# Kernel tuning notes

Hardware: AMD Instinct MI355X
Metric: run time of the kernel (lower is better)

The kernel has to match this reference:

```python
import jax, jax.numpy as jnp
import numpy as np
from math import sqrt

MIN_SCORE = 0.05
MAX_OVERLAP = 0.45
TOP_K = 200


def make_priors():
    feature_dims = {'mid': 18, 'end': 9, 'a': 9, 'b': 5, 'c': 3, 'd': 1}
    obj_scales = {'mid': 0.2, 'end': 0.2, 'a': 0.375, 'b': 0.55, 'c': 0.725, 'd': 0.9}
    aspect_ratio = {'mid': [1.0, 2.0, 3.0, 0.5, 0.333], 'end': [1.0, 2.0, 3.0, 0.5, 0.333],
                    'a': [1.0, 2.0, 3.0, 0.5, 0.333], 'b': [1.0, 2.0, 3.0, 0.5, 0.333],
                    'c': [1.0, 2.0, 0.5], 'd': [1.0, 2.0, 0.5]}
    fmaps = list(feature_dims.keys())
    boxes = []
    for k, fmap in enumerate(fmaps):
        for i in range(feature_dims[fmap]):
            for j in range(feature_dims[fmap]):
                cx = (j + 0.5) / feature_dims[fmap]
                cy = (i + 0.5) / feature_dims[fmap]
                for ratio in aspect_ratio[fmap]:
                    boxes.append([cx, cy, obj_scales[fmap] * sqrt(ratio), obj_scales[fmap] / sqrt(ratio)])
                if fmap in ['mid', 'end', 'a', 'b', 'c']:
                    s = sqrt(obj_scales[fmap] * obj_scales[fmaps[k + 1]])
                else:
                    s = 1.0
                boxes.append([cx, cy, s, s])
    return np.clip(np.asarray(boxes, dtype=np.float32), 0.0, 1.0)  # [3106, 4]


def setup_inputs() -> dict:
    key = jax.random.key(0)
    k1, k2 = jax.random.split(key)
    return {
        'predicted_locs': jax.random.normal(k1, (4, 3106, 4), dtype=jnp.float32),
        'predicted_scores': jax.random.normal(k2, (4, 3106, 21), dtype=jnp.float32),
        'priors_cxcy': jnp.asarray(make_priors()),
    }


def _decode(predicted_locs, priors):
    # gcxgcy_to_cxcy then cxcy_to_xy (standard SSD variances 0.1 / 0.2)
    cxcy = predicted_locs[..., :2] * priors[..., 2:] / 10.0 + priors[..., :2]
    wh = jnp.exp(predicted_locs[..., 2:] / 5.0) * priors[..., 2:]
    return jnp.concatenate([cxcy - wh / 2.0, cxcy + wh / 2.0], axis=-1)  # xyxy


def _detect_image(boxes_i, probs_i):
    # boxes_i: [P,4] xyxy, probs_i: [P,C] softmax scores
    P = boxes_i.shape[0]
    C = probs_i.shape[1]
    # full pairwise Jaccard overlap [P,P]
    lt = jnp.maximum(boxes_i[:, None, :2], boxes_i[None, :, :2])
    rb = jnp.minimum(boxes_i[:, None, 2:], boxes_i[None, :, 2:])
    inter = jnp.prod(jnp.clip(rb - lt, 0.0), axis=-1)
    area = jnp.prod(boxes_i[:, 2:] - boxes_i[:, :2], axis=-1)
    iou = inter / (area[:, None] + area[None, :] - inter)

    cls = probs_i[:, 1:].T                      # [C-1, P], skip background
    valid = cls > MIN_SCORE
    order = jnp.argsort(-jnp.where(valid, cls, -jnp.inf), axis=1)  # [C-1, P]
    valid_s = jnp.take_along_axis(valid, order, axis=1)
    iou_sg = jax.lax.stop_gradient(iou)

    def body(i, suppress):                       # greedy NMS over sorted boxes, all classes at once
        bi = order[:, i]                         # [C-1] prior index per class
        rows = jnp.take_along_axis(iou_sg[bi], order, axis=1) > MAX_OVERLAP  # [C-1, P]
        skip = suppress[:, i] | ~valid_s[:, i]
        proc = (suppress | rows).at[:, i].set(False)
        return jnp.where(skip[:, None], suppress, proc)

    suppress = jax.lax.fori_loop(0, P, body, ~valid_s)
    keep = ~suppress                             # [C-1, P] (sorted order)

    scores_s = jnp.take_along_axis(cls, order, axis=1)
    cand_scores = jnp.where(keep, scores_s, -jnp.inf).reshape(-1)     # [(C-1)*P]
    cand_boxes = boxes_i[order].reshape(-1, 4)
    cand_labels = jnp.broadcast_to(jnp.arange(1, C, dtype=jnp.int32)[:, None], (C - 1, P)).reshape(-1)

    top_scores, top_idx = jax.lax.top_k(cand_scores, TOP_K)
    top_boxes = cand_boxes[top_idx]
    top_labels = cand_labels[top_idx]

    has = jnp.isfinite(top_scores)
    top_scores = jnp.where(has, top_scores, 0.0)
    top_boxes = jnp.where(has[:, None], top_boxes, 0.0)
    top_labels = jnp.where(has, top_labels, 0)
    count = jnp.minimum(jnp.sum(keep).astype(jnp.int32), TOP_K)

    # torch fallback: a single background box when nothing is detected
    none = count == 0
    top_boxes = top_boxes.at[0].set(jnp.where(none, jnp.array([0.0, 0.0, 1.0, 1.0], dtype=top_boxes.dtype), top_boxes[0]))
    count = jnp.where(none, jnp.int32(1), count)
    return top_boxes, top_labels, top_scores, count


def reference(predicted_locs, predicted_scores, priors_cxcy):
    probs = jax.nn.softmax(predicted_scores, axis=2)          # [B,P,C]
    boxes = _decode(predicted_locs, priors_cxcy[None])        # [B,P,4]
    all_boxes, all_labels, all_scores, counts = jax.vmap(_detect_image)(boxes, probs)
    return all_boxes, all_labels, all_scores, counts
```

## Files before the change

kernel.cpp:

```cpp
#include <hip/hip_runtime.h>

#define NB 4
#define NPRI 3106
#define NC 21
#define NCLS 20
#define KMAX 200
#define NMAX 1024
#define WMAX 16
#define TMAX (WMAX*(WMAX+1)/2)
#define MIN_SC 0.05f
#define MAX_OV 0.45f

#define F_PROBS 0
#define F_KEYS  (F_PROBS + NB*NCLS*NPRI)
#define F_BOXES (F_KEYS + NB*NCLS*NMAX*2)
#define F_AREAS (F_BOXES + NB*NCLS*NMAX*4)
#define F_NCAND (F_AREAS + NB*NCLS*NMAX)
#define F_M     (F_NCAND + 128)
#define F_POOL  (F_M + NB*NCLS*WMAX*NMAX*2)
#define F_CNT   (F_POOL + NB*NCLS*KMAX*2)
#define F_DONE  (F_CNT + NB*NCLS)

#define OUT_BOXES  0
#define OUT_LABELS (NB*KMAX*4)
#define OUT_SCORES (OUT_LABELS + NB*KMAX)
#define OUT_COUNTS (OUT_SCORES + NB*KMAX)

__device__ __forceinline__ void decode_box(const float* __restrict__ locs,
                                           const float* __restrict__ priors,
                                           int b, int pi,
                                           float& x1, float& y1, float& x2, float& y2) {
    const float* l  = locs + ((size_t)b * NPRI + pi) * 4;
    const float* pr = priors + (size_t)pi * 4;
    float pcx = pr[0], pcy = pr[1], pw = pr[2], ph = pr[3];
    float cx = l[0] * pw / 10.0f + pcx;
    float cy = l[1] * ph / 10.0f + pcy;
    float w  = expf(l[2] / 5.0f) * pw;
    float h  = expf(l[3] / 5.0f) * ph;
    x1 = cx - w / 2.0f;  y1 = cy - h / 2.0f;
    x2 = cx + w / 2.0f;  y2 = cy + h / 2.0f;
}

__device__ __forceinline__ unsigned long long shfl_xor_u64(unsigned long long v, int m) {
    unsigned lo = (unsigned)v, hi = (unsigned)(v >> 32);
    lo = __shfl_xor(lo, m);
    hi = __shfl_xor(hi, m);
    return ((unsigned long long)hi << 32) | lo;
}

__device__ __forceinline__ void softmax_push(const float* __restrict__ v, int c,
                                             int r, unsigned long long* keys,
                                             int* n_sh) {
    float m = -1e30f;
    #pragma unroll
    for (int k = 0; k < NC; ++k) m = fmaxf(m, v[k]);
    float sum = 0.0f, ec = 0.0f;
    #pragma unroll
    for (int k = 0; k < NC; ++k) {
        float e = expf(v[k] - m);
        sum += e;
        if (k == c + 1) ec = e;
    }
    float val = ec / sum;
    if (val > MIN_SC) {
        int idx = atomicAdd(n_sh, 1);
        if (idx < NMAX) {
            unsigned int sb = __float_as_uint(val);
            keys[idx] = ((unsigned long long)(~sb) << 32) | (unsigned int)r;
        }
    }
}

__global__ __launch_bounds__(1024)
void det_prep(const float* __restrict__ scores, const float* __restrict__ locs,
              const float* __restrict__ priors, float* __restrict__ ws) {
    const int bc  = blockIdx.x;
    const int b   = bc / NCLS;
    const int c   = bc - b * NCLS;
    const int tid = threadIdx.x;

    __shared__ unsigned long long keys[NMAX];
    __shared__ int n_sh;
    if (tid == 0) n_sh = 0;
    __syncthreads();

    const float* sbase = scores + (size_t)b * NPRI * NC;
    {
        float v0[NC], v1[NC], v2[NC];
        const float* s0 = sbase + (size_t)(tid)        * NC;
        const float* s1 = sbase + (size_t)(tid + 1024) * NC;
        const float* s2 = sbase + (size_t)(tid + 2048) * NC;
        #pragma unroll
        for (int k = 0; k < NC; ++k) { v0[k] = s0[k]; }
        #pragma unroll
        for (int k = 0; k < NC; ++k) { v1[k] = s1[k]; }
        #pragma unroll
        for (int k = 0; k < NC; ++k) { v2[k] = s2[k]; }
        softmax_push(v0, c, tid,        keys, &n_sh);
        softmax_push(v1, c, tid + 1024, keys, &n_sh);
        softmax_push(v2, c, tid + 2048, keys, &n_sh);
        if (tid < NPRI - 3072) {
            float v3[NC];
            const float* s3 = sbase + (size_t)(tid + 3072) * NC;
            #pragma unroll
            for (int k = 0; k < NC; ++k) { v3[k] = s3[k]; }
            softmax_push(v3, c, tid + 3072, keys, &n_sh);
        }
    }
    __syncthreads();
    int n = n_sh; if (n > NMAX) n = NMAX;

    unsigned long long mykey = (tid < n) ? keys[tid] : ~0ull;
    __syncthreads();
    for (int k = 2; k <= NMAX; k <<= 1) {
        for (int j = k >> 1; j > 0; j >>= 1) {
            unsigned long long other;
            if (j >= 64) {
                keys[tid] = mykey;
                __syncthreads();
                other = keys[tid ^ j];
                __syncthreads();
            } else {
                other = shfl_xor_u64(mykey, j);
            }
            bool lower    = (tid & j) == 0;
            bool up       = (tid & k) == 0;
            bool take_min = (lower == up);
            bool swap     = take_min ? (other < mykey) : (other > mykey);
            mykey = swap ? other : mykey;
        }
    }

    if (tid == 0) ((int*)(ws + F_NCAND))[bc] = n;
    unsigned long long* gk = (unsigned long long*)(ws + F_KEYS) + (size_t)bc * NMAX;
    float4* gb = (float4*)(ws + F_BOXES) + (size_t)bc * NMAX;
    float*  ga = ws + F_AREAS + (size_t)bc * NMAX;
    if (tid < n) {
        gk[tid] = mykey;
        int pi = (int)(mykey & 0xFFFFFFFFull);
        float x1, y1, x2, y2;
        decode_box(locs, priors, b, pi, x1, y1, x2, y2);
        gb[tid] = make_float4(x1, y1, x2, y2);
        ga[tid] = (x2 - x1) * (y2 - y1);
    }
}

__global__ __launch_bounds__(256)
void det_mbuild(float* __restrict__ ws) {
    const int bc = blockIdx.y;
    const int t  = blockIdx.x * 4 + (threadIdx.x >> 6);
    if (t >= TMAX) return;
    const int wv   = threadIdx.x >> 6;
    const int lane = threadIdx.x & 63;
    int tj = 0;
    while ((tj + 1) * (tj + 2) / 2 <= t) ++tj;
    const int w = t - tj * (tj + 1) / 2;
    const int n = ((const int*)(ws + F_NCAND))[bc];
    const int bi0 = w * 64, bj0 = tj * 64;
    if (bj0 >= n) return;

    __shared__ float4 wbox[4][64];
    __shared__ float  warea[4][64];

    const float4* bx = (const float4*)(ws + F_BOXES) + (size_t)bc * NMAX;
    const float*  ar = ws + F_AREAS + (size_t)bc * NMAX;
    const float4 bi = bx[bi0 + lane];
    const float  ai = ar[bi0 + lane];
    wbox[wv][lane]  = bx[bj0 + lane];
    warea[wv][lane] = ar[bj0 + lane];
    const unsigned long long vm =
        (n - bi0 >= 64) ? ~0ull : ((1ull << (n - bi0)) - 1ull);
    const bool diag = (w == tj);
    unsigned long long myword = 0ull;

    const float4* __restrict__ jb = wbox[wv];
    const float*  __restrict__ ja = warea[wv];

    #pragma unroll
    for (int jj = 0; jj < 64; jj += 2) {
        float4 ca = jb[jj];
        float  aau = ja[jj];
        float4 cb = jb[jj + 1];
        float  bau = ja[jj + 1];

        float alx = fmaxf(bi.x, ca.x), aly = fmaxf(bi.y, ca.y);
        float arx = fminf(bi.z, ca.z), ary = fminf(bi.w, ca.w);
        float blx = fmaxf(bi.x, cb.x), bly = fmaxf(bi.y, cb.y);
        float brx = fminf(bi.z, cb.z), bry = fminf(bi.w, cb.w);
        float adx = fmaxf(arx - alx, 0.0f), ady = fmaxf(ary - aly, 0.0f);
        float bdx = fmaxf(brx - blx, 0.0f), bdy = fmaxf(bry - bly, 0.0f);
        float ain = adx * ady;
        float bin = bdx * bdy;
        float au  = ai + aau - ain;
        float bu  = ai + bau - bin;
        float at  = MAX_OV * au;
        float bt  = MAX_OV * bu;
        bool akeep = ain > at;
        bool bkeep = bin > bt;
        bool anear = fabsf(ain - at) <= at * 6e-7f;
        bool bnear = fabsf(bin - bt) <= bt * 6e-7f;
        if (__ballot(anear || bnear)) {
            float aio = ain / au;
            float bio = bin / bu;
            akeep = anear ? (aio > MAX_OV) : akeep;
            bkeep = bnear ? (bio > MAX_OV) : bkeep;
        }
        unsigned long long abits = __ballot(akeep) & vm;
        unsigned long long bbits = __ballot(bkeep) & vm;
        if (diag) {
            abits &= (1ull << jj) - 1ull;
            bbits &= (1ull << (jj + 1)) - 1ull;
        }
        if (lane == jj)     myword = abits;
        if (lane == jj + 1) myword = bbits;
    }
    if (bj0 + lane < n)
        ((unsigned long long*)(ws + F_M))
            [((size_t)bc * WMAX + w) * NMAX + bj0 + lane] = myword;
}

__global__ __launch_bounds__(256)
void det_finishA(float* __restrict__ ws, float* __restrict__ out) {
    const int bc   = blockIdx.x;
    const int b    = bc / NCLS;
    const int c    = bc - b * NCLS;
    const int cls  = c + 1;
    const int tid  = threadIdx.x;

    if (tid < 64) {
        const int lane = tid;
        const int n    = ((const int*)(ws + F_NCAND))[bc];
        const unsigned long long* Mb =
            (const unsigned long long*)(ws + F_M) + (size_t)bc * WMAX * NMAX;

        unsigned long long kw[WMAX];
        #pragma unroll
        for (int w = 0; w < WMAX; ++w) kw[w] = 0ull;

        const unsigned long long lmask = (1ull << lane) - 1ull;
        #pragma unroll
        for (int w = 0; w < WMAX; ++w) {
            if (w * 64 < n) {
                int cc = w * 64 + lane;
                bool valid = cc < n;
                unsigned long long pre = 0ull;
                #pragma unroll
                for (int v = 0; v < WMAX; ++v)
                    if (v < w) pre |= Mb[(size_t)v * NMAX + cc] & kw[v];
                unsigned long long dg = Mb[(size_t)w * NMAX + cc] & lmask;
                bool sup0 = (pre != 0ull);
                unsigned long long K = __ballot(valid && !sup0);
                for (int it = 0; it < 64; ++it) {
                    bool sup = sup0 || ((dg & K) != 0ull);
                    unsigned long long Kn = __ballot(valid && !sup);
                    if (Kn == K) break;
                    K = Kn;
                }
                kw[w] = K;
            }
        }

        int pref[WMAX + 1];
        pref[0] = 0;
        #pragma unroll
        for (int w = 0; w < WMAX; ++w) pref[w + 1] = pref[w] + __popcll(kw[w]);
        if (lane == 0) ((int*)(ws + F_CNT))[bc] = pref[WMAX];

        const unsigned long long* gk =
            (const unsigned long long*)(ws + F_KEYS) + (size_t)bc * NMAX;
        unsigned long long* pool =
            (unsigned long long*)(ws + F_POOL) + (size_t)bc * KMAX;
        const unsigned long long ctag = (unsigned long long)(cls << 12);
        #pragma unroll
        for (int w = 0; w < WMAX; ++w) {
            unsigned long long kwv = kw[w];
            int cc = w * 64 + lane;
            if (cc < n && ((kwv >> lane) & 1ull)) {
                int pos = pref[w] + __popcll(kwv & lmask);
                if (pos < KMAX) pool[pos] = gk[cc] | ctag;
            }
        }
    }

    {
        int idx = c * 256 + tid;
        if (idx < KMAX * 4) {
            out[OUT_BOXES + (size_t)b * KMAX * 4 + idx] = 0.0f;
        } else if (idx < KMAX * 4 + KMAX) {
            out[OUT_LABELS + b * KMAX + (idx - KMAX * 4)] = 0.0f;
        } else if (idx < KMAX * 4 + 2 * KMAX) {
            out[OUT_SCORES + b * KMAX + (idx - KMAX * 4 - KMAX)] = 0.0f;
        }
    }
}

__global__ __launch_bounds__(256)
void det_finishB(const float* __restrict__ locs, const float* __restrict__ priors,
                 const float* __restrict__ ws, float* __restrict__ out) {
    const int bc   = blockIdx.x;
    const int b    = bc / NCLS;
    const int c    = bc - b * NCLS;
    const int tid  = threadIdx.x;

    __shared__ unsigned long long lpool[NCLS * KMAX];
    __shared__ int cnts[NCLS];

    const int* cnt = (const int*)(ws + F_CNT);
    if (tid < NCLS) cnts[tid] = cnt[b * NCLS + tid];
    __syncthreads();

    const unsigned long long* pool =
        (const unsigned long long*)(ws + F_POOL) + (size_t)b * NCLS * KMAX;
    for (int i = tid; i < NCLS * KMAX; i += 256) {
        int c2 = i / KMAX, r = i - c2 * KMAX;
        int mc2 = cnts[c2] < KMAX ? cnts[c2] : KMAX;
        lpool[i] = (r < mc2) ? pool[i] : ~0ull;
    }
    __syncthreads();

    if (c == 0 && tid == 0) {
        int tot = 0;
        for (int c2 = 0; c2 < NCLS; ++c2) tot += cnts[c2];
        int count = tot < KMAX ? tot : KMAX;
        if (tot == 0) {
            float* ob = out + OUT_BOXES + (size_t)b * KMAX * 4;
            ob[0] = 0.0f; ob[1] = 0.0f; ob[2] = 1.0f; ob[3] = 1.0f;
            count = 1;
        }
        out[OUT_COUNTS + b] = (float)count;
    }

    const int mc = cnts[c] < KMAX ? cnts[c] : KMAX;
    if (tid < mc) {
        unsigned long long key = lpool[c * KMAX + tid];
        int rank = 0;
        #pragma unroll
        for (int c2 = 0; c2 < NCLS; ++c2) {
            int lo = 0, hi = KMAX;
            #pragma unroll
            for (int s = 0; s < 8; ++s) {
                int mid = (lo + hi) >> 1;
                int midc = mid < KMAX ? mid : KMAX - 1;
                unsigned long long v = lpool[c2 * KMAX + midc];
                bool lt = (lo < hi) && (v < key);
                lo = lt ? mid + 1 : lo;
                hi = lt ? hi : mid;
            }
            rank += lo;
        }
        if (rank < KMAX) {
            unsigned int lo32 = (unsigned int)key;
            int pi  = lo32 & 0xFFF;
            int lab = (lo32 >> 12) & 0x1F;
            float sc = __uint_as_float(~(unsigned int)(key >> 32));
            float x1, y1, x2, y2;
            decode_box(locs, priors, b, pi, x1, y1, x2, y2);
            float* ob = out + OUT_BOXES + ((size_t)b * KMAX + rank) * 4;
            ob[0] = x1; ob[1] = y1; ob[2] = x2; ob[3] = y2;
            out[OUT_LABELS + b * KMAX + rank] = (float)lab;
            out[OUT_SCORES + b * KMAX + rank] = sc;
        }
    }
}

extern "C" void kernel_launch(void* const* d_in, const int* in_sizes, int n_in,
                              void* d_out, int out_size, void* d_ws, size_t ws_size,
                              hipStream_t stream) {
    const float* locs   = (const float*)d_in[0];
    const float* scores = (const float*)d_in[1];
    const float* priors = (const float*)d_in[2];
    float* out = (float*)d_out;
    float* ws  = (float*)d_ws;

    det_prep<<<NB * NCLS, 1024, 0, stream>>>(scores, locs, priors, ws);
    det_mbuild<<<dim3((TMAX + 3) / 4, NB * NCLS), 256, 0, stream>>>(ws);
    det_finishA<<<NB * NCLS, 256, 0, stream>>>(ws, out);
    det_finishB<<<NB * NCLS, 256, 0, stream>>>(locs, priors, ws, out);
}
```

Measured before the change: 142.8 us.

## Fuse candidate prep and overlap-matrix build into one split kernel

```diff
diff --git a/kernel.cpp b/kernel.cpp
--- a/kernel.cpp
+++ b/kernel.cpp
@@ -8,6 +8,7 @@
 #define NMAX 1024
 #define WMAX 16
 #define TMAX (WMAX*(WMAX+1)/2)
+#define NSPLIT 3
 #define MIN_SC 0.05f
 #define MAX_OV 0.45f
 
@@ -72,14 +73,19 @@
 }
 
 __global__ __launch_bounds__(1024)
-void det_prep(const float* __restrict__ scores, const float* __restrict__ locs,
-              const float* __restrict__ priors, float* __restrict__ ws) {
-    const int bc  = blockIdx.x;
-    const int b   = bc / NCLS;
-    const int c   = bc - b * NCLS;
-    const int tid = threadIdx.x;
+void det_fused(const float* __restrict__ scores, const float* __restrict__ locs,
+               const float* __restrict__ priors, float* __restrict__ ws) {
+    const int h    = blockIdx.x;
+    const int bc   = blockIdx.y;
+    const int b    = bc / NCLS;
+    const int c    = bc - b * NCLS;
+    const int tid  = threadIdx.x;
+    const int wv   = tid >> 6;
+    const int lane = tid & 63;
 
     __shared__ unsigned long long keys[NMAX];
+    __shared__ float4 bxL[NMAX];
+    __shared__ float  arL[NMAX];
     __shared__ int n_sh;
     if (tid == 0) n_sh = 0;
     __syncthreads();
@@ -131,92 +137,82 @@
         }
     }
 
-    if (tid == 0) ((int*)(ws + F_NCAND))[bc] = n;
-    unsigned long long* gk = (unsigned long long*)(ws + F_KEYS) + (size_t)bc * NMAX;
-    float4* gb = (float4*)(ws + F_BOXES) + (size_t)bc * NMAX;
-    float*  ga = ws + F_AREAS + (size_t)bc * NMAX;
+    if (h == 0) {
+        if (tid == 0) ((int*)(ws + F_NCAND))[bc] = n;
+        if (tid < n)
+            ((unsigned long long*)(ws + F_KEYS))[(size_t)bc * NMAX + tid] = mykey;
+    }
     if (tid < n) {
-        gk[tid] = mykey;
         int pi = (int)(mykey & 0xFFFFFFFFull);
         float x1, y1, x2, y2;
         decode_box(locs, priors, b, pi, x1, y1, x2, y2);
-        gb[tid] = make_float4(x1, y1, x2, y2);
-        ga[tid] = (x2 - x1) * (y2 - y1);
-    }
-}
-
-__global__ __launch_bounds__(256)
-void det_mbuild(float* __restrict__ ws) {
-    const int bc = blockIdx.y;
-    const int t  = blockIdx.x * 4 + (threadIdx.x >> 6);
-    if (t >= TMAX) return;
-    const int wv   = threadIdx.x >> 6;
-    const int lane = threadIdx.x & 63;
-    int tj = 0;
-    while ((tj + 1) * (tj + 2) / 2 <= t) ++tj;
-    const int w = t - tj * (tj + 1) / 2;
-    const int n = ((const int*)(ws + F_NCAND))[bc];
-    const int bi0 = w * 64, bj0 = tj * 64;
-    if (bj0 >= n) return;
-
-    __shared__ float4 wbox[4][64];
-    __shared__ float  warea[4][64];
-
-    const float4* bx = (const float4*)(ws + F_BOXES) + (size_t)bc * NMAX;
-    const float*  ar = ws + F_AREAS + (size_t)bc * NMAX;
-    const float4 bi = bx[bi0 + lane];
-    const float  ai = ar[bi0 + lane];
-    wbox[wv][lane]  = bx[bj0 + lane];
-    warea[wv][lane] = ar[bj0 + lane];
-    const unsigned long long vm =
-        (n - bi0 >= 64) ? ~0ull : ((1ull << (n - bi0)) - 1ull);
-    const bool diag = (w == tj);
-    unsigned long long myword = 0ull;
-
-    const float4* __restrict__ jb = wbox[wv];
-    const float*  __restrict__ ja = warea[wv];
-
-    #pragma unroll
-    for (int jj = 0; jj < 64; jj += 2) {
-        float4 ca = jb[jj];
-        float  aau = ja[jj];
-        float4 cb = jb[jj + 1];
-        float  bau = ja[jj + 1];
-
-        float alx = fmaxf(bi.x, ca.x), aly = fmaxf(bi.y, ca.y);
-        float arx = fminf(bi.z, ca.z), ary = fminf(bi.w, ca.w);
-        float blx = fmaxf(bi.x, cb.x), bly = fmaxf(bi.y, cb.y);
-        float brx = fminf(bi.z, cb.z), bry = fminf(bi.w, cb.w);
-        float adx = fmaxf(arx - alx, 0.0f), ady = fmaxf(ary - aly, 0.0f);
-        float bdx = fmaxf(brx - blx, 0.0f), bdy = fmaxf(bry - bly, 0.0f);
-        float ain = adx * ady;
-        float bin = bdx * bdy;
-        float au  = ai + aau - ain;
-        float bu  = ai + bau - bin;
-        float at  = MAX_OV * au;
-        float bt  = MAX_OV * bu;
-        bool akeep = ain > at;
-        bool bkeep = bin > bt;
-        bool anear = fabsf(ain - at) <= at * 6e-7f;
-        bool bnear = fabsf(bin - bt) <= bt * 6e-7f;
-        if (__ballot(anear || bnear)) {
-            float aio = ain / au;
-            float bio = bin / bu;
-            akeep = anear ? (aio > MAX_OV) : akeep;
-            bkeep = bnear ? (bio > MAX_OV) : bkeep;
-        }
-        unsigned long long abits = __ballot(akeep) & vm;
-        unsigned long long bbits = __ballot(bkeep) & vm;
-        if (diag) {
-            abits &= (1ull << jj) - 1ull;
-            bbits &= (1ull << (jj + 1)) - 1ull;
-        }
-        if (lane == jj)     myword = abits;
-        if (lane == jj + 1) myword = bbits;
-    }
-    if (bj0 + lane < n)
-        ((unsigned long long*)(ws + F_M))
-            [((size_t)bc * WMAX + w) * NMAX + bj0 + lane] = myword;
+        bxL[tid] = make_float4(x1, y1, x2, y2);
+        arL[tid] = (x2 - x1) * (y2 - y1);
+    } else {
+        bxL[tid] = make_float4(0.0f, 0.0f, 0.0f, 0.0f);
+        arL[tid] = 0.0f;
+    }
+    __syncthreads();
+
+    for (int t = h + NSPLIT * wv; t < TMAX; t += NSPLIT * 16) {
+        int tj = 0;
+        while ((tj + 1) * (tj + 2) / 2 <= t) ++tj;
+        const int w = t - tj * (tj + 1) / 2;
+        const int bi0 = w * 64, bj0 = tj * 64;
+        if (bj0 >= n) continue;
+
+        const float4 bi = bxL[bi0 + lane];
+        const float  ai = arL[bi0 + lane];
+        const unsigned long long vm =
+            (n - bi0 >= 64) ? ~0ull : ((1ull << (n - bi0)) - 1ull);
+        const bool diag = (w == tj);
+        unsigned long long myword = 0ull;
+
+        const float4* __restrict__ jb = &bxL[bj0];
+        const float*  __restrict__ ja = &arL[bj0];
+
+        #pragma unroll
+        for (int jj = 0; jj < 64; jj += 2) {
+            float4 ca = jb[jj];
+            float  aau = ja[jj];
+            float4 cb = jb[jj + 1];
+            float  bau = ja[jj + 1];
+
+            float alx = fmaxf(bi.x, ca.x), aly = fmaxf(bi.y, ca.y);
+            float arx = fminf(bi.z, ca.z), ary = fminf(bi.w, ca.w);
+            float blx = fmaxf(bi.x, cb.x), bly = fmaxf(bi.y, cb.y);
+            float brx = fminf(bi.z, cb.z), bry = fminf(bi.w, cb.w);
+            float adx = fmaxf(arx - alx, 0.0f), ady = fmaxf(ary - aly, 0.0f);
+            float bdx = fmaxf(brx - blx, 0.0f), bdy = fmaxf(bry - bly, 0.0f);
+            float ain = adx * ady;
+            float bin = bdx * bdy;
+            float au  = ai + aau - ain;
+            float bu  = ai + bau - bin;
+            float at  = MAX_OV * au;
+            float bt  = MAX_OV * bu;
+            bool akeep = ain > at;
+            bool bkeep = bin > bt;
+            bool anear = fabsf(ain - at) <= at * 6e-7f;
+            bool bnear = fabsf(bin - bt) <= bt * 6e-7f;
+            if (__ballot(anear || bnear)) {
+                float aio = ain / au;
+                float bio = bin / bu;
+                akeep = anear ? (aio > MAX_OV) : akeep;
+                bkeep = bnear ? (bio > MAX_OV) : bkeep;
+            }
+            unsigned long long abits = __ballot(akeep) & vm;
+            unsigned long long bbits = __ballot(bkeep) & vm;
+            if (diag) {
+                abits &= (1ull << jj) - 1ull;
+                bbits &= (1ull << (jj + 1)) - 1ull;
+            }
+            if (lane == jj)     myword = abits;
+            if (lane == jj + 1) myword = bbits;
+        }
+        if (bj0 + lane < n)
+            ((unsigned long long*)(ws + F_M))
+                [((size_t)bc * WMAX + w) * NMAX + bj0 + lane] = myword;
+    }
 }
 
 __global__ __launch_bounds__(256)
@@ -372,8 +368,7 @@
     float* out = (float*)d_out;
     float* ws  = (float*)d_ws;
 
-    det_prep<<<NB * NCLS, 1024, 0, stream>>>(scores, locs, priors, ws);
-    det_mbuild<<<dim3((TMAX + 3) / 4, NB * NCLS), 256, 0, stream>>>(ws);
+    det_fused<<<dim3(NSPLIT, NB * NCLS), 1024, 0, stream>>>(scores, locs, priors, ws);
     det_finishA<<<NB * NCLS, 256, 0, stream>>>(ws, out);
     det_finishB<<<NB * NCLS, 256, 0, stream>>>(locs, priors, ws, out);
 }
```

After: 150.9 us. 1.06x slower.

## Compute softmax once in a separate kernel instead of per class block

Applied to the files above, without the earlier changes.

```diff
diff --git a/kernel.cpp b/kernel.cpp
--- a/kernel.cpp
+++ b/kernel.cpp
@@ -48,35 +48,35 @@
     return ((unsigned long long)hi << 32) | lo;
 }
 
-__device__ __forceinline__ void softmax_push(const float* __restrict__ v, int c,
-                                             int r, unsigned long long* keys,
-                                             int* n_sh) {
+__global__ __launch_bounds__(256)
+void det_softmax(const float* __restrict__ scores, float* __restrict__ ws) {
+    __shared__ float row[256 * NC];
+    const int t0 = blockIdx.x * 256;
+    int items = NB * NPRI - t0; if (items > 256) items = 256;
+    const int cntf = items * NC;
+    for (int i = threadIdx.x; i < cntf; i += 256)
+        row[i] = scores[(size_t)t0 * NC + i];
+    __syncthreads();
+    const int t = t0 + threadIdx.x;
+    if (t >= NB * NPRI) return;
+    const int b = t / NPRI, p = t - b * NPRI;
+    const float* s = row + threadIdx.x * NC;
     float m = -1e30f;
     #pragma unroll
-    for (int k = 0; k < NC; ++k) m = fmaxf(m, v[k]);
-    float sum = 0.0f, ec = 0.0f;
+    for (int c = 0; c < NC; ++c) m = fmaxf(m, s[c]);
+    float e[NC]; float sum = 0.0f;
     #pragma unroll
-    for (int k = 0; k < NC; ++k) {
-        float e = expf(v[k] - m);
-        sum += e;
-        if (k == c + 1) ec = e;
-    }
-    float val = ec / sum;
-    if (val > MIN_SC) {
-        int idx = atomicAdd(n_sh, 1);
-        if (idx < NMAX) {
-            unsigned int sb = __float_as_uint(val);
-            keys[idx] = ((unsigned long long)(~sb) << 32) | (unsigned int)r;
-        }
-    }
+    for (int c = 0; c < NC; ++c) { e[c] = expf(s[c] - m); sum += e[c]; }
+    #pragma unroll
+    for (int c = 1; c < NC; ++c)
+        ws[F_PROBS + ((size_t)(b * NCLS + (c - 1)) * NPRI + p)] = e[c] / sum;
 }
 
 __global__ __launch_bounds__(1024)
-void det_prep(const float* __restrict__ scores, const float* __restrict__ locs,
-              const float* __restrict__ priors, float* __restrict__ ws) {
+void det_prep(const float* __restrict__ locs, const float* __restrict__ priors,
+              float* __restrict__ ws) {
     const int bc  = blockIdx.x;
     const int b   = bc / NCLS;
-    const int c   = bc - b * NCLS;
     const int tid = threadIdx.x;
 
     __shared__ unsigned long long keys[NMAX];
@@ -84,27 +84,15 @@
     if (tid == 0) n_sh = 0;
     __syncthreads();
 
-    const float* sbase = scores + (size_t)b * NPRI * NC;
-    {
-        float v0[NC], v1[NC], v2[NC];
-        const float* s0 = sbase + (size_t)(tid)        * NC;
-        const float* s1 = sbase + (size_t)(tid + 1024) * NC;
-        const float* s2 = sbase + (size_t)(tid + 2048) * NC;
-        #pragma unroll
-        for (int k = 0; k < NC; ++k) { v0[k] = s0[k]; }
-        #pragma unroll
-        for (int k = 0; k < NC; ++k) { v1[k] = s1[k]; }
-        #pragma unroll
-        for (int k = 0; k < NC; ++k) { v2[k] = s2[k]; }
-        softmax_push(v0, c, tid,        keys, &n_sh);
-        softmax_push(v1, c, tid + 1024, keys, &n_sh);
-        softmax_push(v2, c, tid + 2048, keys, &n_sh);
-        if (tid < NPRI - 3072) {
-            float v3[NC];
-            const float* s3 = sbase + (size_t)(tid + 3072) * NC;
-            #pragma unroll
-            for (int k = 0; k < NC; ++k) { v3[k] = s3[k]; }
-            softmax_push(v3, c, tid + 3072, keys, &n_sh);
+    const float* prob = ws + F_PROBS + (size_t)bc * NPRI;
+    for (int p = tid; p < NPRI; p += 1024) {
+        float s = prob[p];
+        if (s > MIN_SC) {
+            int idx = atomicAdd(&n_sh, 1);
+            if (idx < NMAX) {
+                unsigned int sb = __float_as_uint(s);
+                keys[idx] = ((unsigned long long)(~sb) << 32) | (unsigned int)p;
+            }
         }
     }
     __syncthreads();
@@ -372,7 +360,8 @@
     float* out = (float*)d_out;
     float* ws  = (float*)d_ws;
 
-    det_prep<<<NB * NCLS, 1024, 0, stream>>>(scores, locs, priors, ws);
+    det_softmax<<<(NB * NPRI + 255) / 256, 256, 0, stream>>>(scores, ws);
+    det_prep<<<NB * NCLS, 1024, 0, stream>>>(locs, priors, ws);
     det_mbuild<<<dim3((TMAX + 3) / 4, NB * NCLS), 256, 0, stream>>>(ws);
     det_finishA<<<NB * NCLS, 256, 0, stream>>>(ws, out);
     det_finishB<<<NB * NCLS, 256, 0, stream>>>(locs, priors, ws, out);
```

New measurement: 140.3 us, median of 3. Within noise of the previous version (-1.7%).
